# Kernel optimization log

Measured on AMD Instinct MI355X. Metric: run time of the kernel, lower is better.

Reference implementation:

```python
import jax, jax.numpy as jnp
import numpy as np

N = 8192
NFEAT = 512
NHID = 256
NCLASS = 128


def setup_inputs() -> dict:
    key = jax.random.key(0)
    k1, k2, k3, k4 = jax.random.split(key, 4)
    feature_s = jax.random.normal(k1, (N, NFEAT), dtype=jnp.float32)
    feature_t = jax.random.normal(k2, (N, NFEAT), dtype=jnp.float32)
    # nn.Linear(in, out, bias=False) weight has shape [out, in]
    w1 = jax.random.normal(k3, (NHID, NFEAT), dtype=jnp.float32) * (1.0 / np.sqrt(NFEAT))
    w2 = jax.random.normal(k4, (NCLASS, NHID), dtype=jnp.float32) * (1.0 / np.sqrt(NHID))
    return {"feature_s": feature_s, "feature_t": feature_t, "w1": w1, "w2": w2}


def reference(feature_s, feature_t, w1, w2):
    # adj = softmax(feature_s @ feature_t^T) over rows (dim=1)
    adj = jax.nn.softmax(feature_s @ feature_t.T, axis=1)  # [N, N]
    # GCN layer 1: linear(adj @ x) with x = feature_s
    x1 = (adj @ feature_s) @ w1.T  # [N, NHID]
    # GCN layer 2
    x2 = (adj @ x1) @ w2.T  # [N, NCLASS]
    return (x1, x2)
```

## Files before the change

### kernel.cpp

```cpp
#include <hip/hip_runtime.h>
#include <stdint.h>


typedef unsigned short u16;
typedef short bf16x8 __attribute__((ext_vector_type(8)));
typedef _Float16 f16x8 __attribute__((ext_vector_type(8)));
typedef float f32x4 __attribute__((ext_vector_type(4)));

#define EPI_STOREB 0
#define EPI_PARTH  1

__device__ __forceinline__ u16 f2bf(float f) {
  unsigned u = __float_as_uint(f);
  u += 0x7fffu + ((u >> 16) & 1u);
  return (u16)(u >> 16);
}
__device__ __forceinline__ u16 f2h(float f) {
  union { _Float16 h; u16 u; } cv; cv.h = (_Float16)f; return cv.u;
}
__device__ __forceinline__ float h2f(u16 u) {
  union { u16 u; _Float16 h; } cv; cv.u = u; return (float)cv.h;
}
__device__ __forceinline__ int swz8(int r) { return (r ^ (r >> 3)) & 7; }

__device__ __forceinline__ void async16(const void* g, void* lds) {
  __builtin_amdgcn_global_load_lds(
      (const __attribute__((address_space(1))) unsigned int*)g,
      (__attribute__((address_space(3))) unsigned int*)lds, 16, 0, 0);
}

__global__ void probe_layout(int* __restrict__ rmap, int* __restrict__ cmap) {
  const int lane = threadIdx.x & 63;
  const int t = lane & 15, quad = lane >> 4;
  bf16x8 avt, av1;
  const u16 bt = f2bf((float)t), b1 = 0x3f80;
#pragma unroll
  for (int j = 0; j < 8; ++j) { ((u16*)&avt)[j] = bt; ((u16*)&av1)[j] = b1; }
  f32x4 z = {0.f, 0.f, 0.f, 0.f};
  f32x4 r1 = __builtin_amdgcn_mfma_f32_16x16x32_bf16(avt, av1, z, 0, 0, 0);
  f32x4 r2 = __builtin_amdgcn_mfma_f32_16x16x32_bf16(av1, avt, z, 0, 0, 0);
  if (threadIdx.x < 64) {
#pragma unroll
    for (int e = 0; e < 4; ++e) {
      int r = (int)(r1[e] * 0.03125f + 0.5f);
      int c = (int)(r2[e] * 0.03125f + 0.5f);
      if (r < 0 || r > 15) r = quad * 4 + e;
      if (c < 0 || c > 15) c = t;
      rmap[lane * 4 + e] = r;
      cmap[lane * 4 + e] = c;
    }
  }
}

__global__ __launch_bounds__(256) void conv_all(
    const float* __restrict__ Fs, const float* __restrict__ Ft,
    const float* __restrict__ W1, const float* __restrict__ W2,
    u16* __restrict__ Fsf, u16* __restrict__ Ftf,
    u16* __restrict__ W1f, u16* __restrict__ W2h) {
  const int bx = blockIdx.x, tid = threadIdx.x;
  if (bx < 2048) {
    for (int i = bx * 256 + tid; i < 4194304; i += 2048 * 256) Fsf[i] = f2h(Fs[i]);
  } else if (bx < 4096) {
    for (int i = (bx - 2048) * 256 + tid; i < 4194304; i += 2048 * 256) Ftf[i] = f2h(Ft[i]);
  } else if (bx < 4160) {
    for (int i = (bx - 4096) * 256 + tid; i < 131072; i += 64 * 256) W1f[i] = f2h(W1[i]);
  } else {
    for (int i = (bx - 4160) * 256 + tid; i < 32768; i += 16 * 256) W2h[i] = f2bf(W2[i]);
  }
}

__global__ __launch_bounds__(256) void gemm_pexp_f16(
    const u16* __restrict__ A, const u16* __restrict__ B, int K, int N,
    u16* __restrict__ P, float* __restrict__ rsp,
    const int* __restrict__ rmap, const int* __restrict__ cmap) {
  __shared__ __align__(16) u16 lA[128 * 64];
  __shared__ __align__(16) u16 lB[128 * 64];
  __shared__ float lrs[128][2];

  const int tid = threadIdx.x;
  const int wave = tid >> 6, lane = tid & 63;
  const int quad = lane >> 4, t = lane & 15;
  const int bm = blockIdx.y * 128, bn = blockIdx.x * 128;
  const int wm = (wave & 1) * 64, wn = (wave >> 1) * 64;

  f32x4 acc[4][4];
#pragma unroll
  for (int i = 0; i < 4; ++i)
#pragma unroll
    for (int j = 0; j < 4; ++j) acc[i][j] = (f32x4){0.f, 0.f, 0.f, 0.f};

  const int srow = tid >> 3, schk = tid & 7;
  const u16* pA[4]; const u16* pB[4];
#pragma unroll
  for (int j = 0; j < 4; ++j) {
    const int r = j * 32 + srow;
    const int c = schk ^ swz8(r);
    pA[j] = A + (size_t)(bm + r) * K + c * 8;
    pB[j] = B + (size_t)(bn + r) * K + c * 8;
  }

  int aoffx[4], boffx[4];
#pragma unroll
  for (int i = 0; i < 4; ++i) {
    const int rm = wm + i * 16 + t;
    aoffx[i] = rm * 128 + (swz8(rm) << 4);
    const int rn = wn + i * 16 + t;
    boffx[i] = rn * 128 + (swz8(rn) << 4);
  }
  const int sq0 = quad << 4, sq1 = (quad << 4) | 64;

  for (int k0 = 0; k0 < K; k0 += 64) {
#pragma unroll
    for (int j = 0; j < 4; ++j) {
      async16(pA[j], (char*)lA + j * 4096 + wave * 1024);
      async16(pB[j], (char*)lB + j * 4096 + wave * 1024);
      pA[j] += 64; pB[j] += 64;
    }
    __syncthreads();
#pragma unroll
    for (int s = 0; s < 2; ++s) {
      const int sq = s ? sq1 : sq0;
      f16x8 av[4], bv[4];
#pragma unroll
      for (int i = 0; i < 4; ++i) {
        av[i] = *(const f16x8*)((const char*)lA + (aoffx[i] ^ sq));
        bv[i] = *(const f16x8*)((const char*)lB + (boffx[i] ^ sq));
      }
#pragma unroll
      for (int mi = 0; mi < 4; ++mi)
#pragma unroll
        for (int ni = 0; ni < 4; ++ni)
          acc[mi][ni] = __builtin_amdgcn_mfma_f32_16x16x32_f16(av[mi], bv[ni], acc[mi][ni], 0, 0, 0);
    }
    __syncthreads();
  }

  int rl[4], cl[4];
#pragma unroll
  for (int e = 0; e < 4; ++e) {
    rl[e] = rmap[lane * 4 + e];
    cl[e] = cmap[lane * 4 + e];
  }
#pragma unroll
  for (int mi = 0; mi < 4; ++mi)
#pragma unroll
    for (int e = 0; e < 4; ++e) {
      const int rloc = wm + mi * 16 + rl[e];
      const int row = bm + rloc;
      float s = 0.f;
#pragma unroll
      for (int ni = 0; ni < 4; ++ni) {
        float p = __expf(acc[mi][ni][e] - 100.0f);
        s += p;
        P[(size_t)row * N + (bn + wn + ni * 16 + cl[e])] = f2bf(p);
      }
      s += __shfl_xor(s, 1, 64);
      s += __shfl_xor(s, 2, 64);
      s += __shfl_xor(s, 4, 64);
      s += __shfl_xor(s, 8, 64);
      if (t == 0) lrs[rloc][wave >> 1] = s;
    }
  __syncthreads();
  if (tid < 128)
    rsp[(size_t)blockIdx.x * 8192 + bm + tid] = lrs[tid][0] + lrs[tid][1];
}

__global__ __launch_bounds__(256) void finalize_invl(
    const float* __restrict__ rsp, float* __restrict__ invl) {
  const int row = blockIdx.x * 256 + threadIdx.x;
  float s = 0.f;
#pragma unroll 8
  for (int b = 0; b < 64; ++b) s += rsp[(size_t)b * 8192 + row];
  invl[row] = 1.0f / s;
}

template <int EPI, int F16>
__global__ __launch_bounds__(256) void gemm_nt(
    const u16* __restrict__ A, const u16* __restrict__ B, int K, int Kc, int N,
    u16* __restrict__ outp, const float* __restrict__ invl,
    const int* __restrict__ rmap, const int* __restrict__ cmap) {
  __shared__ __align__(16) u16 lA[128 * 64];
  __shared__ __align__(16) u16 lB[128 * 64];

  const int tid = threadIdx.x;
  const int wave = tid >> 6, lane = tid & 63;
  const int quad = lane >> 4, t = lane & 15;
  const int bm = blockIdx.y * 128, bn = blockIdx.x * 128;
  const int wm = (wave & 1) * 64, wn = (wave >> 1) * 64;
  const int koff = blockIdx.z * Kc;

  f32x4 acc[4][4];
#pragma unroll
  for (int i = 0; i < 4; ++i)
#pragma unroll
    for (int j = 0; j < 4; ++j) acc[i][j] = (f32x4){0.f, 0.f, 0.f, 0.f};

  const int srow = tid >> 3, schk = tid & 7;
  const u16* pA[4]; const u16* pB[4];
#pragma unroll
  for (int j = 0; j < 4; ++j) {
    const int r = j * 32 + srow;
    const int c = schk ^ swz8(r);
    pA[j] = A + (size_t)(bm + r) * K + koff + c * 8;
    pB[j] = B + (size_t)(bn + r) * K + koff + c * 8;
  }

  int aoffx[4], boffx[4];
#pragma unroll
  for (int i = 0; i < 4; ++i) {
    const int rm = wm + i * 16 + t;
    aoffx[i] = rm * 128 + (swz8(rm) << 4);
    const int rn = wn + i * 16 + t;
    boffx[i] = rn * 128 + (swz8(rn) << 4);
  }
  const int sq0 = quad << 4, sq1 = (quad << 4) | 64;

  for (int k0 = 0; k0 < Kc; k0 += 64) {
#pragma unroll
    for (int j = 0; j < 4; ++j) {
      async16(pA[j], (char*)lA + j * 4096 + wave * 1024);
      async16(pB[j], (char*)lB + j * 4096 + wave * 1024);
      pA[j] += 64; pB[j] += 64;
    }
    __syncthreads();
#pragma unroll
    for (int s = 0; s < 2; ++s) {
      const int sq = s ? sq1 : sq0;
      bf16x8 av[4], bv[4];
#pragma unroll
      for (int i = 0; i < 4; ++i) {
        av[i] = *(const bf16x8*)((const char*)lA + (aoffx[i] ^ sq));
        bv[i] = *(const bf16x8*)((const char*)lB + (boffx[i] ^ sq));
      }
#pragma unroll
      for (int mi = 0; mi < 4; ++mi)
#pragma unroll
        for (int ni = 0; ni < 4; ++ni) {
          if constexpr (F16)
            acc[mi][ni] = __builtin_amdgcn_mfma_f32_16x16x32_f16(
                __builtin_bit_cast(f16x8, av[mi]), __builtin_bit_cast(f16x8, bv[ni]),
                acc[mi][ni], 0, 0, 0);
          else
            acc[mi][ni] = __builtin_amdgcn_mfma_f32_16x16x32_bf16(av[mi], bv[ni], acc[mi][ni], 0, 0, 0);
        }
    }
    __syncthreads();
  }

  int rl[4], cl[4];
#pragma unroll
  for (int e = 0; e < 4; ++e) {
    rl[e] = rmap[lane * 4 + e];
    cl[e] = cmap[lane * 4 + e];
  }
  const size_t zoff = (size_t)blockIdx.z * ((size_t)gridDim.y * 128) * N;
#pragma unroll
  for (int mi = 0; mi < 4; ++mi)
#pragma unroll
    for (int e = 0; e < 4; ++e) {
      const int row = bm + wm + mi * 16 + rl[e];
      const float sc = (EPI == EPI_PARTH) ? invl[row] : 1.0f;
#pragma unroll
      for (int ni = 0; ni < 4; ++ni) {
        const size_t idx = (size_t)row * N + (bn + wn + ni * 16 + cl[e]);
        if (EPI == EPI_PARTH) outp[zoff + idx] = f2h(acc[mi][ni][e] * sc);
        else                  outp[idx] = f2bf(acc[mi][ni][e]);
      }
    }
}

__global__ __launch_bounds__(256) void combine1(
    const u16* __restrict__ pp, const float* __restrict__ invl,
    float* __restrict__ x1f, u16* __restrict__ x1h) {
  const int row = blockIdx.x, j = threadIdx.x;
  const size_t i = (size_t)row * 256 + j;
  const float v = h2f(pp[i]) + h2f(pp[2097152 + i]) +
                  h2f(pp[4194304 + i]) + h2f(pp[6291456 + i]);
  x1f[i] = v;
  x1h[i] = f2bf(v);
}

__global__ __launch_bounds__(128) void combine2(
    const u16* __restrict__ pp, const float* __restrict__ invl,
    float* __restrict__ x2f) {
  const int row = blockIdx.x, j = threadIdx.x;
  const size_t i = (size_t)row * 128 + j;
  float s = 0.f;
#pragma unroll
  for (int z = 0; z < 8; ++z) s += h2f(pp[(size_t)z * 1048576 + i]);
  x2f[i] = s;
}

extern "C" void kernel_launch(void* const* d_in, const int* in_sizes, int n_in,
                              void* d_out, int out_size, void* d_ws, size_t ws_size,
                              hipStream_t stream) {
  const float* Fs = (const float*)d_in[0];
  const float* Ft = (const float*)d_in[1];
  const float* W1 = (const float*)d_in[2];
  const float* W2 = (const float*)d_in[3];

  char* ws = (char*)d_ws;
  u16*   P    = (u16*)(ws);
  u16*   Fsf  = (u16*)(ws + 134217728);
  u16*   Ftf  = (u16*)(ws + 142606336);
  u16*   pp   = (u16*)(ws + 134217728);
  float* rsp  = (float*)(ws + 150994944);
  u16*   Y1T  = (u16*)(ws + 153091200);
  u16*   x1h  = (u16*)(ws + 157286400);
  u16*   Y2T  = (u16*)(ws + 161480704);
  float* invl = (float*)(ws + 163577856);
  int*   rmap = (int*)  (ws + 163610624);
  int*   cmap = (int*)  (ws + 163611648);
  u16*   W1f  = (u16*)(ws + 163612672);
  u16*   W2h  = (u16*)(ws + 163874816);

  float* x1f = (float*)d_out;
  float* x2f = (float*)d_out + 2097152;

  dim3 blk(256);
  probe_layout<<<1, 64, 0, stream>>>(rmap, cmap);
  conv_all<<<4176, blk, 0, stream>>>(Fs, Ft, W1, W2, Fsf, Ftf, W1f, W2h);
  gemm_pexp_f16<<<dim3(64, 64), blk, 0, stream>>>(Fsf, Ftf, 512, 8192, P, rsp, rmap, cmap);
  finalize_invl<<<32, blk, 0, stream>>>(rsp, invl);
  gemm_nt<EPI_STOREB, 1><<<dim3(64, 2), blk, 0, stream>>>(W1f, Fsf, 512, 512, 8192,
                                                          Y1T, nullptr, rmap, cmap);
  gemm_nt<EPI_PARTH, 0><<<dim3(2, 64, 4), blk, 0, stream>>>(P, Y1T, 8192, 2048, 256,
                                                            pp, invl, rmap, cmap);
  combine1<<<8192, blk, 0, stream>>>(pp, invl, x1f, x1h);
  gemm_nt<EPI_STOREB, 0><<<dim3(64, 1), blk, 0, stream>>>(W2h, x1h, 256, 256, 8192,
                                                          Y2T, nullptr, rmap, cmap);
  gemm_nt<EPI_PARTH, 0><<<dim3(1, 64, 8), blk, 0, stream>>>(P, Y2T, 8192, 1024, 128,
                                                            pp, invl, rmap, cmap);
  combine2<<<8192, dim3(128), 0, stream>>>(pp, invl, x2f);
}
```

Before: 308.6 us.

## Vectorize conversions, enlarge QK tile to 512 rows, use K=128 stages for adj GEMMs

The fp32-to-half conversion kernel now handles four elements per thread using float4 loads and packed stores. The QK^T exp GEMM now uses 1024-thread blocks with 512x128 tiles, so each B tile is shared by more A rows, and it reuses the A shared buffer for the row-sum reduction. The big P@Y GEMMs move to a dedicated kernel that stages 128-wide K chunks with a 16-way XOR swizzle, halving the number of barrier rounds. In exchange, shared memory per block and block size grow, which may reduce occupancy, and there is still no double buffering.

```diff
diff --git a/kernel.cpp b/kernel.cpp
--- a/kernel.cpp
+++ b/kernel.cpp
@@ -52,36 +52,55 @@
   }
 }
 
+__device__ __forceinline__ void cvt4h(const float4* in, uint2* out, int i) {
+  float4 v = in[i];
+  uint2 o;
+  o.x = (unsigned)f2h(v.x) | ((unsigned)f2h(v.y) << 16);
+  o.y = (unsigned)f2h(v.z) | ((unsigned)f2h(v.w) << 16);
+  out[i] = o;
+}
+__device__ __forceinline__ void cvt4b(const float4* in, uint2* out, int i) {
+  float4 v = in[i];
+  uint2 o;
+  o.x = (unsigned)f2bf(v.x) | ((unsigned)f2bf(v.y) << 16);
+  o.y = (unsigned)f2bf(v.z) | ((unsigned)f2bf(v.w) << 16);
+  out[i] = o;
+}
+
 __global__ __launch_bounds__(256) void conv_all(
     const float* __restrict__ Fs, const float* __restrict__ Ft,
     const float* __restrict__ W1, const float* __restrict__ W2,
     u16* __restrict__ Fsf, u16* __restrict__ Ftf,
     u16* __restrict__ W1f, u16* __restrict__ W2h) {
   const int bx = blockIdx.x, tid = threadIdx.x;
-  if (bx < 2048) {
-    for (int i = bx * 256 + tid; i < 4194304; i += 2048 * 256) Fsf[i] = f2h(Fs[i]);
-  } else if (bx < 4096) {
-    for (int i = (bx - 2048) * 256 + tid; i < 4194304; i += 2048 * 256) Ftf[i] = f2h(Ft[i]);
-  } else if (bx < 4160) {
-    for (int i = (bx - 4096) * 256 + tid; i < 131072; i += 64 * 256) W1f[i] = f2h(W1[i]);
+  if (bx < 1024) {
+    for (int i = bx * 256 + tid; i < 1048576; i += 1024 * 256)
+      cvt4h((const float4*)Fs, (uint2*)Fsf, i);
+  } else if (bx < 2048) {
+    for (int i = (bx - 1024) * 256 + tid; i < 1048576; i += 1024 * 256)
+      cvt4h((const float4*)Ft, (uint2*)Ftf, i);
+  } else if (bx < 2080) {
+    for (int i = (bx - 2048) * 256 + tid; i < 32768; i += 32 * 256)
+      cvt4h((const float4*)W1, (uint2*)W1f, i);
   } else {
-    for (int i = (bx - 4160) * 256 + tid; i < 32768; i += 16 * 256) W2h[i] = f2bf(W2[i]);
-  }
-}
-
-__global__ __launch_bounds__(256) void gemm_pexp_f16(
+    for (int i = (bx - 2080) * 256 + tid; i < 8192; i += 8 * 256)
+      cvt4b((const float4*)W2, (uint2*)W2h, i);
+  }
+}
+
+__global__ __launch_bounds__(1024) void gemm_pexp_f16_512(
     const u16* __restrict__ A, const u16* __restrict__ B, int K, int N,
     u16* __restrict__ P, float* __restrict__ rsp,
     const int* __restrict__ rmap, const int* __restrict__ cmap) {
-  __shared__ __align__(16) u16 lA[128 * 64];
+  __shared__ __align__(16) u16 lA[512 * 64];
   __shared__ __align__(16) u16 lB[128 * 64];
-  __shared__ float lrs[128][2];
+  float* lrs = (float*)lA;
 
   const int tid = threadIdx.x;
   const int wave = tid >> 6, lane = tid & 63;
   const int quad = lane >> 4, t = lane & 15;
-  const int bm = blockIdx.y * 128, bn = blockIdx.x * 128;
-  const int wm = (wave & 1) * 64, wn = (wave >> 1) * 64;
+  const int bm = blockIdx.y * 512, bn = blockIdx.x * 128;
+  const int wm = (wave & 7) * 64, wn = (wave >> 3) * 64;
 
   f32x4 acc[4][4];
 #pragma unroll
@@ -90,14 +109,13 @@
     for (int j = 0; j < 4; ++j) acc[i][j] = (f32x4){0.f, 0.f, 0.f, 0.f};
 
   const int srow = tid >> 3, schk = tid & 7;
-  const u16* pA[4]; const u16* pB[4];
+  const u16* pA[4]; const u16* pB0;
 #pragma unroll
   for (int j = 0; j < 4; ++j) {
-    const int r = j * 32 + srow;
-    const int c = schk ^ swz8(r);
-    pA[j] = A + (size_t)(bm + r) * K + c * 8;
-    pB[j] = B + (size_t)(bn + r) * K + c * 8;
-  }
+    const int r = j * 128 + srow;
+    pA[j] = A + (size_t)(bm + r) * K + (schk ^ swz8(r)) * 8;
+  }
+  pB0 = B + (size_t)(bn + srow) * K + (schk ^ swz8(srow)) * 8;
 
   int aoffx[4], boffx[4];
 #pragma unroll
@@ -112,10 +130,11 @@
   for (int k0 = 0; k0 < K; k0 += 64) {
 #pragma unroll
     for (int j = 0; j < 4; ++j) {
-      async16(pA[j], (char*)lA + j * 4096 + wave * 1024);
-      async16(pB[j], (char*)lB + j * 4096 + wave * 1024);
-      pA[j] += 64; pB[j] += 64;
-    }
+      async16(pA[j], (char*)lA + j * 16384 + wave * 1024);
+      pA[j] += 64;
+    }
+    async16(pB0, (char*)lB + wave * 1024);
+    pB0 += 64;
     __syncthreads();
 #pragma unroll
     for (int s = 0; s < 2; ++s) {
@@ -158,11 +177,11 @@
       s += __shfl_xor(s, 2, 64);
       s += __shfl_xor(s, 4, 64);
       s += __shfl_xor(s, 8, 64);
-      if (t == 0) lrs[rloc][wave >> 1] = s;
+      if (t == 0) lrs[rloc * 2 + (wave >> 3)] = s;
     }
   __syncthreads();
-  if (tid < 128)
-    rsp[(size_t)blockIdx.x * 8192 + bm + tid] = lrs[tid][0] + lrs[tid][1];
+  if (tid < 512)
+    rsp[(size_t)blockIdx.x * 8192 + bm + tid] = lrs[tid * 2] + lrs[tid * 2 + 1];
 }
 
 __global__ __launch_bounds__(256) void finalize_invl(
@@ -174,13 +193,12 @@
   invl[row] = 1.0f / s;
 }
 
-template <int EPI, int F16>
-__global__ __launch_bounds__(256) void gemm_nt(
+__global__ __launch_bounds__(256) void gemm_nt128(
     const u16* __restrict__ A, const u16* __restrict__ B, int K, int Kc, int N,
     u16* __restrict__ outp, const float* __restrict__ invl,
     const int* __restrict__ rmap, const int* __restrict__ cmap) {
-  __shared__ __align__(16) u16 lA[128 * 64];
-  __shared__ __align__(16) u16 lB[128 * 64];
+  __shared__ __align__(16) u16 lA[128 * 128];
+  __shared__ __align__(16) u16 lB[128 * 128];
 
   const int tid = threadIdx.x;
   const int wave = tid >> 6, lane = tid & 63;
@@ -195,14 +213,100 @@
 #pragma unroll
     for (int j = 0; j < 4; ++j) acc[i][j] = (f32x4){0.f, 0.f, 0.f, 0.f};
 
+  const int srow = tid >> 4, schk = tid & 15;
+  const int scol = (schk ^ srow) * 8;
+  const u16* pA[8]; const u16* pB[8];
+#pragma unroll
+  for (int j = 0; j < 8; ++j) {
+    pA[j] = A + (size_t)(bm + j * 16 + srow) * K + koff + scol;
+    pB[j] = B + (size_t)(bn + j * 16 + srow) * K + koff + scol;
+  }
+
+  int abase[4], bbase[4], arx[4], brx[4];
+#pragma unroll
+  for (int i = 0; i < 4; ++i) {
+    const int rm = wm + i * 16 + t;
+    abase[i] = rm * 256; arx[i] = rm & 15;
+    const int rn = wn + i * 16 + t;
+    bbase[i] = rn * 256; brx[i] = rn & 15;
+  }
+
+  const int iters = Kc >> 7;
+  for (int it = 0; it < iters; ++it) {
+#pragma unroll
+    for (int j = 0; j < 8; ++j) {
+      async16(pA[j], (char*)lA + j * 4096 + wave * 1024);
+      async16(pB[j], (char*)lB + j * 4096 + wave * 1024);
+      pA[j] += 128; pB[j] += 128;
+    }
+    __syncthreads();
+#pragma unroll
+    for (int s = 0; s < 4; ++s) {
+      const int c = (s << 2) | quad;
+      bf16x8 av[4], bv[4];
+#pragma unroll
+      for (int i = 0; i < 4; ++i) {
+        av[i] = *(const bf16x8*)((const char*)lA + abase[i] + ((c ^ arx[i]) << 4));
+        bv[i] = *(const bf16x8*)((const char*)lB + bbase[i] + ((c ^ brx[i]) << 4));
+      }
+#pragma unroll
+      for (int mi = 0; mi < 4; ++mi)
+#pragma unroll
+        for (int ni = 0; ni < 4; ++ni)
+          acc[mi][ni] = __builtin_amdgcn_mfma_f32_16x16x32_bf16(av[mi], bv[ni], acc[mi][ni], 0, 0, 0);
+    }
+    __syncthreads();
+  }
+
+  int rl[4], cl[4];
+#pragma unroll
+  for (int e = 0; e < 4; ++e) {
+    rl[e] = rmap[lane * 4 + e];
+    cl[e] = cmap[lane * 4 + e];
+  }
+  const size_t zoff = (size_t)blockIdx.z * ((size_t)gridDim.y * 128) * N;
+#pragma unroll
+  for (int mi = 0; mi < 4; ++mi)
+#pragma unroll
+    for (int e = 0; e < 4; ++e) {
+      const int row = bm + wm + mi * 16 + rl[e];
+      const float sc = invl[row];
+#pragma unroll
+      for (int ni = 0; ni < 4; ++ni) {
+        const size_t idx = (size_t)row * N + (bn + wn + ni * 16 + cl[e]);
+        outp[zoff + idx] = f2h(acc[mi][ni][e] * sc);
+      }
+    }
+}
+
+template <int F16>
+__global__ __launch_bounds__(256) void gemm_nt(
+    const u16* __restrict__ A, const u16* __restrict__ B, int K, int N,
+    u16* __restrict__ outp,
+    const int* __restrict__ rmap, const int* __restrict__ cmap) {
+  __shared__ __align__(16) u16 lA[128 * 64];
+  __shared__ __align__(16) u16 lB[128 * 64];
+
+  const int tid = threadIdx.x;
+  const int wave = tid >> 6, lane = tid & 63;
+  const int quad = lane >> 4, t = lane & 15;
+  const int bm = blockIdx.y * 128, bn = blockIdx.x * 128;
+  const int wm = (wave & 1) * 64, wn = (wave >> 1) * 64;
+
+  f32x4 acc[4][4];
+#pragma unroll
+  for (int i = 0; i < 4; ++i)
+#pragma unroll
+    for (int j = 0; j < 4; ++j) acc[i][j] = (f32x4){0.f, 0.f, 0.f, 0.f};
+
   const int srow = tid >> 3, schk = tid & 7;
   const u16* pA[4]; const u16* pB[4];
 #pragma unroll
   for (int j = 0; j < 4; ++j) {
     const int r = j * 32 + srow;
     const int c = schk ^ swz8(r);
-    pA[j] = A + (size_t)(bm + r) * K + koff + c * 8;
-    pB[j] = B + (size_t)(bn + r) * K + koff + c * 8;
+    pA[j] = A + (size_t)(bm + r) * K + c * 8;
+    pB[j] = B + (size_t)(bn + r) * K + c * 8;
   }
 
   int aoffx[4], boffx[4];
@@ -215,7 +319,7 @@
   }
   const int sq0 = quad << 4, sq1 = (quad << 4) | 64;
 
-  for (int k0 = 0; k0 < Kc; k0 += 64) {
+  for (int k0 = 0; k0 < K; k0 += 64) {
 #pragma unroll
     for (int j = 0; j < 4; ++j) {
       async16(pA[j], (char*)lA + j * 4096 + wave * 1024);
@@ -253,19 +357,14 @@
     rl[e] = rmap[lane * 4 + e];
     cl[e] = cmap[lane * 4 + e];
   }
-  const size_t zoff = (size_t)blockIdx.z * ((size_t)gridDim.y * 128) * N;
 #pragma unroll
   for (int mi = 0; mi < 4; ++mi)
 #pragma unroll
     for (int e = 0; e < 4; ++e) {
       const int row = bm + wm + mi * 16 + rl[e];
-      const float sc = (EPI == EPI_PARTH) ? invl[row] : 1.0f;
-#pragma unroll
-      for (int ni = 0; ni < 4; ++ni) {
-        const size_t idx = (size_t)row * N + (bn + wn + ni * 16 + cl[e]);
-        if (EPI == EPI_PARTH) outp[zoff + idx] = f2h(acc[mi][ni][e] * sc);
-        else                  outp[idx] = f2bf(acc[mi][ni][e]);
-      }
+#pragma unroll
+      for (int ni = 0; ni < 4; ++ni)
+        outp[(size_t)row * N + (bn + wn + ni * 16 + cl[e])] = f2bf(acc[mi][ni][e]);
     }
 }
 
@@ -319,17 +418,16 @@
 
   dim3 blk(256);
   probe_layout<<<1, 64, 0, stream>>>(rmap, cmap);
-  conv_all<<<4176, blk, 0, stream>>>(Fs, Ft, W1, W2, Fsf, Ftf, W1f, W2h);
-  gemm_pexp_f16<<<dim3(64, 64), blk, 0, stream>>>(Fsf, Ftf, 512, 8192, P, rsp, rmap, cmap);
+  conv_all<<<2088, blk, 0, stream>>>(Fs, Ft, W1, W2, Fsf, Ftf, W1f, W2h);
+  gemm_pexp_f16_512<<<dim3(64, 16), dim3(1024), 0, stream>>>(
+      Fsf, Ftf, 512, 8192, P, rsp, rmap, cmap);
   finalize_invl<<<32, blk, 0, stream>>>(rsp, invl);
-  gemm_nt<EPI_STOREB, 1><<<dim3(64, 2), blk, 0, stream>>>(W1f, Fsf, 512, 512, 8192,
-                                                          Y1T, nullptr, rmap, cmap);
-  gemm_nt<EPI_PARTH, 0><<<dim3(2, 64, 4), blk, 0, stream>>>(P, Y1T, 8192, 2048, 256,
-                                                            pp, invl, rmap, cmap);
+  gemm_nt<1><<<dim3(64, 2), blk, 0, stream>>>(W1f, Fsf, 512, 8192, Y1T, rmap, cmap);
+  gemm_nt128<<<dim3(2, 64, 4), blk, 0, stream>>>(P, Y1T, 8192, 2048, 256,
+                                                 pp, invl, rmap, cmap);
   combine1<<<8192, blk, 0, stream>>>(pp, invl, x1f, x1h);
-  gemm_nt<EPI_STOREB, 0><<<dim3(64, 1), blk, 0, stream>>>(W2h, x1h, 256, 256, 8192,
-                                                          Y2T, nullptr, rmap, cmap);
-  gemm_nt<EPI_PARTH, 0><<<dim3(1, 64, 8), blk, 0, stream>>>(P, Y2T, 8192, 1024, 128,
-                                                            pp, invl, rmap, cmap);
+  gemm_nt<0><<<dim3(64, 1), blk, 0, stream>>>(W2h, x1h, 256, 8192, Y2T, rmap, cmap);
+  gemm_nt128<<<dim3(1, 64, 8), blk, 0, stream>>>(P, Y2T, 8192, 1024, 128,
+                                                 pp, invl, rmap, cmap);
   combine2<<<8192, dim3(128), 0, stream>>>(pp, invl, x2f);
 }
```

After: 320.2 us. +3.7%, slower.
